# Optimization experiments

Hardware: AMD Instinct MI355X
Metric: run time of the kernel (lower is better)

## Reference

```python
import jax, jax.numpy as jnp
import numpy as np

B, C, N = 8, 512, 2048
C8 = C // 8


def setup_inputs() -> dict:
    key = jax.random.key(0)
    kx, kq, kk, kv, kg = jax.random.split(key, 5)
    return {
        "x": jax.random.normal(kx, (B, C, N), dtype=jnp.float32),
        "Wq": jax.random.normal(kq, (C8, C), dtype=jnp.float32) * (1.0 / np.sqrt(C)),
        "Wk": jax.random.normal(kk, (C8, C), dtype=jnp.float32) * (1.0 / np.sqrt(C)),
        "Wv": jax.random.normal(kv, (C, C), dtype=jnp.float32) * (1.0 / np.sqrt(C)),
        # torch init is gamma=0.0; use a small random value so the attention
        # branch contributes to the output.
        "gamma": jax.random.uniform(kg, (1,), dtype=jnp.float32),
    }


def reference(x, Wq, Wk, Wv, gamma):
    # 1x1 convs == per-position linear maps over channels
    f = jnp.einsum("oc,bcn->bon", Wq, x)   # [B, C/8, N]
    g = jnp.einsum("oc,bcn->bon", Wk, x)   # [B, C/8, N]
    h = jnp.einsum("oc,bcn->bon", Wv, x)   # [B, C,   N]
    # scores[b,n,m] = sum_c f[b,c,n] * g[b,c,m]  (unscaled, as in source)
    scores = jnp.einsum("bcn,bcm->bnm", f, g)  # [B, N, N]
    # softmax over dim=1 (the query-position axis) — atypical but faithful
    beta = jax.nn.softmax(scores, axis=1)
    # o = gamma * h @ beta + x
    o = gamma[0] * jnp.einsum("bcn,bnm->bcm", h, beta) + x
    return o
```

## Files before the change

### kernel.cpp

```cpp
#include <hip/hip_runtime.h>
#include <hip/hip_bf16.h>
#include <math.h>

#define NB 8
#define NC 512
#define NN 2048

typedef unsigned short u16;
typedef __attribute__((ext_vector_type(8))) short short8;
typedef __attribute__((ext_vector_type(4))) float f32x4;

__device__ __forceinline__ float bf16_to_f32(u16 v) {
  union { unsigned int u; float f; } c; c.u = ((unsigned int)v) << 16; return c.f;
}
__device__ __forceinline__ u16 f32_to_bf16(float f) {
  __hip_bfloat16 h = __float2bfloat16(f);
  union { __hip_bfloat16 h; u16 u; } c; c.h = h; return c.u;
}
__device__ __forceinline__ void split2(float v, unsigned short& hi, unsigned short& lo) {
  hi = f32_to_bf16(v);
  lo = f32_to_bf16(v - bf16_to_f32(hi));
}

__device__ __forceinline__ void gl_lds16(const void* g, void* l) {
  __builtin_amdgcn_global_load_lds(
      (const __attribute__((address_space(1))) unsigned int*)g,
      (__attribute__((address_space(3))) unsigned int*)l, 16, 0, 0);
}

__device__ __forceinline__ void stage128x32(const u16* __restrict__ src, size_t row_base,
                                            int selems, int k0, u16* lds, int tid) {
#pragma unroll
  for (int s = 0; s < 2; ++s) {
    int flat = s * 4096 + tid * 16;
    int row = flat >> 6;
    int kb  = flat & 63;
    const char* g = (const char*)(src + (row_base + row) * (size_t)selems + k0) + kb;
    u16* l = lds + s * 2048 + (tid & ~63) * 8;
    gl_lds16(g, l);
  }
}

__global__ __launch_bounds__(256)
void wsplit_kernel(const float* __restrict__ Wq, const float* __restrict__ Wk,
                   const float* __restrict__ Wv, u16* __restrict__ Whi,
                   u16* __restrict__ Wlo) {
  int idx = (blockIdx.x * 256 + threadIdx.x) * 4;
  int r = idx >> 9, c = idx & 511;
  const float* src;
  if (r < 64)       src = Wq + (size_t)r * NC + c;
  else if (r < 128) src = Wk + (size_t)(r - 64) * NC + c;
  else              src = Wv + (size_t)(r - 128) * NC + c;
  float4 v = *(const float4*)src;
  ushort4 hi, lo;
  split2(v.x, hi.x, lo.x); split2(v.y, hi.y, lo.y);
  split2(v.z, hi.z, lo.z); split2(v.w, hi.w, lo.w);
  *(ushort4*)&Whi[idx] = hi;
  *(ushort4*)&Wlo[idx] = lo;
}

__global__ __launch_bounds__(256)
void xsplit_kernel(const float* __restrict__ x, u16* __restrict__ xThi,
                   u16* __restrict__ xTlo) {
  const int b = blockIdx.z, c0 = blockIdx.y * 64, n0 = blockIdx.x * 64;
  __shared__ float t[64][65];
  const int tid = threadIdx.x, tx = tid & 15, ty = tid >> 4;
#pragma unroll
  for (int r = 0; r < 4; ++r) {
    int c = r * 16 + ty;
    float4 v = *(const float4*)&x[((size_t)b * NC + c0 + c) * NN + n0 + tx * 4];
    t[c][tx * 4 + 0] = v.x; t[c][tx * 4 + 1] = v.y;
    t[c][tx * 4 + 2] = v.z; t[c][tx * 4 + 3] = v.w;
  }
  __syncthreads();
#pragma unroll
  for (int r = 0; r < 4; ++r) {
    int n = r * 16 + ty;
    ushort4 hi, lo;
    split2(t[tx * 4 + 0][n], hi.x, lo.x);
    split2(t[tx * 4 + 1][n], hi.y, lo.y);
    split2(t[tx * 4 + 2][n], hi.z, lo.z);
    split2(t[tx * 4 + 3][n], hi.w, lo.w);
    size_t off = ((size_t)b * NN + n0 + n) * NC + c0 + tx * 4;
    *(ushort4*)&xThi[off] = hi;
    *(ushort4*)&xTlo[off] = lo;
  }
}

__global__ __launch_bounds__(256)
void proj_mfma_kernel(const u16* __restrict__ xThi, const u16* __restrict__ xTlo,
                      const u16* __restrict__ Whi, const u16* __restrict__ Wlo,
                      u16* __restrict__ fgThi, u16* __restrict__ fgTlo,
                      u16* __restrict__ hw) {
  const int b  = blockIdx.z;
  const int n0 = blockIdx.x * 128;
  const int r0 = blockIdx.y * 128;
  const bool fg = (r0 == 0);

  __shared__ u16 Wh[2][128 * 32], Wl[2][128 * 32], Xh[2][128 * 32], Xl[2][128 * 32];

  const int tid = threadIdx.x, wave = tid >> 6, lane = tid & 63;
  const int quad = lane >> 4, l16 = lane & 15;
  const int wa = (wave >> 1) * 64, wb = (wave & 1) * 64;
  const size_t xrow = (size_t)b * NN + n0;

  f32x4 acc[4][4];
#pragma unroll
  for (int i = 0; i < 4; ++i)
#pragma unroll
    for (int j = 0; j < 4; ++j) acc[i][j] = (f32x4){0.f, 0.f, 0.f, 0.f};

  stage128x32(Whi, r0, NC, 0, Wh[0], tid);
  stage128x32(xThi, xrow, NC, 0, Xh[0], tid);
  if (fg) {
    stage128x32(Wlo, r0, NC, 0, Wl[0], tid);
    stage128x32(xTlo, xrow, NC, 0, Xl[0], tid);
  }

  const int KIT = NC / 32;
  for (int ki = 0; ki < KIT; ++ki) {
    __syncthreads();
    if (ki + 1 < KIT) {
      const int nb = (ki + 1) & 1, k1 = (ki + 1) * 32;
      stage128x32(Whi, r0, NC, k1, Wh[nb], tid);
      stage128x32(xThi, xrow, NC, k1, Xh[nb], tid);
      if (fg) {
        stage128x32(Wlo, r0, NC, k1, Wl[nb], tid);
        stage128x32(xTlo, xrow, NC, k1, Xl[nb], tid);
      }
    }
    const int cur = ki & 1;

    if (fg) {
      short8 ah[4], al[4], bh[4], bl[4];
#pragma unroll
      for (int i = 0; i < 4; ++i) {
        ah[i] = *(short8*)&Wh[cur][(wa + i * 16 + l16) * 32 + quad * 8];
        al[i] = *(short8*)&Wl[cur][(wa + i * 16 + l16) * 32 + quad * 8];
      }
#pragma unroll
      for (int j = 0; j < 4; ++j) {
        bh[j] = *(short8*)&Xh[cur][(wb + j * 16 + l16) * 32 + quad * 8];
        bl[j] = *(short8*)&Xl[cur][(wb + j * 16 + l16) * 32 + quad * 8];
      }
#pragma unroll
      for (int i = 0; i < 4; ++i)
#pragma unroll
        for (int j = 0; j < 4; ++j) {
          acc[i][j] = __builtin_amdgcn_mfma_f32_16x16x32_bf16(ah[i], bh[j], acc[i][j], 0, 0, 0);
          acc[i][j] = __builtin_amdgcn_mfma_f32_16x16x32_bf16(ah[i], bl[j], acc[i][j], 0, 0, 0);
          acc[i][j] = __builtin_amdgcn_mfma_f32_16x16x32_bf16(al[i], bh[j], acc[i][j], 0, 0, 0);
        }
    } else {
      short8 ah[4], bh[4];
#pragma unroll
      for (int i = 0; i < 4; ++i)
        ah[i] = *(short8*)&Xh[cur][(wa + i * 16 + l16) * 32 + quad * 8];
#pragma unroll
      for (int j = 0; j < 4; ++j)
        bh[j] = *(short8*)&Wh[cur][(wb + j * 16 + l16) * 32 + quad * 8];
#pragma unroll
      for (int i = 0; i < 4; ++i)
#pragma unroll
        for (int j = 0; j < 4; ++j)
          acc[i][j] = __builtin_amdgcn_mfma_f32_16x16x32_bf16(ah[i], bh[j], acc[i][j], 0, 0, 0);
    }
  }

  if (fg) {
#pragma unroll
    for (int i = 0; i < 4; ++i)
#pragma unroll
      for (int j = 0; j < 4; ++j) {
        int rb = wa + i * 16 + quad * 4;
        int n  = n0 + wb + j * 16 + l16;
        ushort4 hi, lo;
        split2(acc[i][j][0], hi.x, lo.x); split2(acc[i][j][1], hi.y, lo.y);
        split2(acc[i][j][2], hi.z, lo.z); split2(acc[i][j][3], hi.w, lo.w);
        size_t off = ((size_t)b * NN + n) * 128 + rb;
        *(ushort4*)&fgThi[off] = hi;
        *(ushort4*)&fgTlo[off] = lo;
      }
  } else {
#pragma unroll
    for (int i = 0; i < 4; ++i)
#pragma unroll
      for (int j = 0; j < 4; ++j) {
        int nb = n0 + wa + i * 16 + quad * 4;
        int c  = r0 - 128 + wb + j * 16 + l16;
        ushort4 hi;
        hi.x = f32_to_bf16(acc[i][j][0]); hi.y = f32_to_bf16(acc[i][j][1]);
        hi.z = f32_to_bf16(acc[i][j][2]); hi.w = f32_to_bf16(acc[i][j][3]);
        *(ushort4*)&hw[((size_t)b * NC + c) * NN + nb] = hi;
      }
  }
}

__global__ __launch_bounds__(512, 2)
void attn_out_kernel(const u16* __restrict__ fgThi, const u16* __restrict__ fgTlo,
                     const u16* __restrict__ hw, const float* __restrict__ x,
                     const float* __restrict__ gamma, float* __restrict__ out) {
  const int s = blockIdx.x;
  const int b = s & 7;
  const int mt = s >> 3;
  const int m0 = mt * 64;

  __shared__ u16 Fh[2][64 * 64], Fl[2][64 * 64];
  __shared__ u16 Ps[64 * 64];
  float* Dn = (float*)Ps;

  const int tid = threadIdx.x, wave = tid >> 6, lane = tid & 63;
  const int quad = lane >> 4, l16 = lane & 15;
  const int ws_n = (wave >> 2) * 32, ws_m = (wave & 3) * 16;
  const int wv_c = wave * 64;

  const size_t frow = (size_t)b * NN;
  const size_t hbase = (size_t)b * NC;

  short8 gh[2], gl[2];
#pragma unroll
  for (int k = 0; k < 2; ++k) {
    size_t o = (frow + m0 + ws_m + l16) * 128 + 64 + k * 32 + quad * 8;
    gh[k] = *(const short8*)&fgThi[o];
    gl[k] = *(const short8*)&fgTlo[o];
  }

  {
    int flat = tid * 16;
    int row = flat >> 7, chunk = (flat >> 4) & 7;
    int kb = ((chunk ^ (row & 7)) << 4);
    gl_lds16((const char*)(fgThi + (frow + row) * 128) + kb, Fh[0] + (tid & ~63) * 8);
    gl_lds16((const char*)(fgTlo + (frow + row) * 128) + kb, Fl[0] + (tid & ~63) * 8);
  }
  __syncthreads();

  float dsum = 0.f;
  f32x4 ao[4][4];
#pragma unroll
  for (int i = 0; i < 4; ++i)
#pragma unroll
    for (int j = 0; j < 4; ++j) ao[i][j] = (f32x4){0.f, 0.f, 0.f, 0.f};

  const int NT = NN / 64;
  for (int it = 0; it < NT; ++it) {
    const int cur = it & 1;
    const int n1 = it * 64;

    short8 hreg[8];
#pragma unroll
    for (int i = 0; i < 4; ++i)
#pragma unroll
      for (int k = 0; k < 2; ++k)
        hreg[i * 2 + k] = *(const short8*)&hw[
            (hbase + wv_c + i * 16 + l16) * NN + n1 + (k * 4 + quad) * 8];

    if (it + 1 < NT) {
      const int nf = (it + 1) * 64;
      int flat = tid * 16;
      int row = flat >> 7, chunk = (flat >> 4) & 7;
      int kb = ((chunk ^ (row & 7)) << 4);
      gl_lds16((const char*)(fgThi + (frow + nf + row) * 128) + kb,
               Fh[cur ^ 1] + (tid & ~63) * 8);
      gl_lds16((const char*)(fgTlo + (frow + nf + row) * 128) + kb,
               Fl[cur ^ 1] + (tid & ~63) * 8);
    }

    f32x4 as[2];
#pragma unroll
    for (int i = 0; i < 2; ++i) as[i] = (f32x4){0.f, 0.f, 0.f, 0.f};
#pragma unroll
    for (int k = 0; k < 2; ++k) {
      short8 fh[2], fl[2];
#pragma unroll
      for (int i = 0; i < 2; ++i) {
        int rr = ws_n + i * 16 + l16;
        int ci = (((k * 4 + quad) ^ (rr & 7)) << 3);
        fh[i] = *(short8*)&Fh[cur][rr * 64 + ci];
        fl[i] = *(short8*)&Fl[cur][rr * 64 + ci];
      }
#pragma unroll
      for (int i = 0; i < 2; ++i) {
        as[i] = __builtin_amdgcn_mfma_f32_16x16x32_bf16(fh[i], gh[k], as[i], 0, 0, 0);
        as[i] = __builtin_amdgcn_mfma_f32_16x16x32_bf16(fh[i], gl[k], as[i], 0, 0, 0);
        as[i] = __builtin_amdgcn_mfma_f32_16x16x32_bf16(fl[i], gh[k], as[i], 0, 0, 0);
      }
    }

    {
      int m = ws_m + l16;
#pragma unroll
      for (int i = 0; i < 2; ++i) {
        float e0 = __expf(as[i][0]);
        float e1 = __expf(as[i][1]);
        float e2 = __expf(as[i][2]);
        float e3 = __expf(as[i][3]);
        dsum += (e0 + e1) + (e2 + e3);
        ushort4 pk;
        pk.x = f32_to_bf16(e0); pk.y = f32_to_bf16(e1);
        pk.z = f32_to_bf16(e2); pk.w = f32_to_bf16(e3);
        int nb = ws_n * 2 + i * 32 + quad * 8;
        int chunk = nb >> 4;
        int off = (nb & 15) >> 1;
        *(ushort4*)&Ps[m * 64 + ((chunk ^ (m & 7)) << 3) + off] = pk;
      }
    }

    asm volatile("s_waitcnt lgkmcnt(0)" ::: "memory");
    __builtin_amdgcn_s_barrier();

#pragma unroll
    for (int k = 0; k < 2; ++k) {
      short8 pb[4];
#pragma unroll
      for (int j = 0; j < 4; ++j) {
        int rm = j * 16 + l16;
        pb[j] = *(short8*)&Ps[rm * 64 + ((((k * 4 + quad)) ^ (rm & 7)) << 3)];
      }
#pragma unroll
      for (int i = 0; i < 4; ++i)
#pragma unroll
        for (int j = 0; j < 4; ++j)
          ao[i][j] = __builtin_amdgcn_mfma_f32_16x16x32_bf16(hreg[i * 2 + k], pb[j], ao[i][j], 0, 0, 0);
    }

    __syncthreads();
  }

  dsum += __shfl_xor(dsum, 16);
  dsum += __shfl_xor(dsum, 32);
  if (tid < 64) Dn[tid] = 0.f;
  __syncthreads();
  if (quad == 0) atomicAdd(&Dn[ws_m + l16], dsum);
  __syncthreads();

  const float g = gamma[0];
  float invd[4];
#pragma unroll
  for (int j = 0; j < 4; ++j)
    invd[j] = g / Dn[j * 16 + l16];

#pragma unroll
  for (int i = 0; i < 4; ++i) {
#pragma unroll
    for (int j = 0; j < 4; ++j) {
      const int c = wv_c + i * 16 + quad * 4;
      const int m = m0 + j * 16 + l16;
#pragma unroll
      for (int r = 0; r < 4; ++r) {
        size_t off = ((size_t)b * NC + c + r) * NN + m;
        out[off] = fmaf(invd[j], ao[i][j][r], x[off]);
      }
    }
  }
}

extern "C" void kernel_launch(void* const* d_in, const int* in_sizes, int n_in,
                              void* d_out, int out_size, void* d_ws, size_t ws_size,
                              hipStream_t stream) {
  const float* x     = (const float*)d_in[0];
  const float* Wq    = (const float*)d_in[1];
  const float* Wk    = (const float*)d_in[2];
  const float* Wv    = (const float*)d_in[3];
  const float* gamma = (const float*)d_in[4];
  float* out = (float*)d_out;

  char* ws = (char*)d_ws;
  u16*   xThi  = (u16*)ws;
  u16*   xTlo  = (u16*)(ws + 16777216);
  u16*   Whi   = (u16*)(ws + 33554432);
  u16*   Wlo   = (u16*)(ws + 34209792);
  u16*   fgThi = (u16*)(ws + 67108864);
  u16*   fgTlo = (u16*)(ws + 71303168);
  u16*   hw    = (u16*)(ws + 75497472);

  wsplit_kernel<<<dim3(320), 256, 0, stream>>>(Wq, Wk, Wv, Whi, Wlo);
  xsplit_kernel<<<dim3(NN / 64, NC / 64, NB), 256, 0, stream>>>(x, xThi, xTlo);
  proj_mfma_kernel<<<dim3(NN / 128, 5, NB), 256, 0, stream>>>(
      xThi, xTlo, Whi, Wlo, fgThi, fgTlo, hw);
  attn_out_kernel<<<dim3(256), 512, 0, stream>>>(fgThi, fgTlo, hw, x, gamma, out);
}
```

Before: 224.0 us.

## Halve attention output tile to 32 columns and double grid size

The attention-output kernel now processes 32 output positions per block instead of 64 and launches 512 blocks instead of 256. Wave roles in the score computation are remapped so each wave computes one 16x16 score tile. The launch-bounds occupancy hint is raised to 4 blocks per CU. The aim is to fill more CUs and hide latency, at the cost of reloading the full F tiles and H rows twice as often per output column, which doubles global traffic for those operands.

```diff
diff --git a/kernel.cpp b/kernel.cpp
--- a/kernel.cpp
+++ b/kernel.cpp
@@ -196,22 +196,22 @@
   }
 }
 
-__global__ __launch_bounds__(512, 2)
+__global__ __launch_bounds__(512, 4)
 void attn_out_kernel(const u16* __restrict__ fgThi, const u16* __restrict__ fgTlo,
                      const u16* __restrict__ hw, const float* __restrict__ x,
                      const float* __restrict__ gamma, float* __restrict__ out) {
   const int s = blockIdx.x;
   const int b = s & 7;
   const int mt = s >> 3;
-  const int m0 = mt * 64;
+  const int m0 = mt * 32;
 
   __shared__ u16 Fh[2][64 * 64], Fl[2][64 * 64];
-  __shared__ u16 Ps[64 * 64];
-  float* Dn = (float*)Ps;
+  __shared__ u16 Ps[32 * 64];
+  __shared__ float Dn[32];
 
   const int tid = threadIdx.x, wave = tid >> 6, lane = tid & 63;
   const int quad = lane >> 4, l16 = lane & 15;
-  const int ws_n = (wave >> 2) * 32, ws_m = (wave & 3) * 16;
+  const int ws_n = (wave >> 1) * 16, ws_m = (wave & 1) * 16;
   const int wv_c = wave * 64;
 
   const size_t frow = (size_t)b * NN;
@@ -235,11 +235,11 @@
   __syncthreads();
 
   float dsum = 0.f;
-  f32x4 ao[4][4];
+  f32x4 ao[4][2];
 #pragma unroll
   for (int i = 0; i < 4; ++i)
 #pragma unroll
-    for (int j = 0; j < 4; ++j) ao[i][j] = (f32x4){0.f, 0.f, 0.f, 0.f};
+    for (int j = 0; j < 2; ++j) ao[i][j] = (f32x4){0.f, 0.f, 0.f, 0.f};
 
   const int NT = NN / 64;
   for (int it = 0; it < NT; ++it) {
@@ -265,44 +265,32 @@
                Fl[cur ^ 1] + (tid & ~63) * 8);
     }
 
-    f32x4 as[2];
-#pragma unroll
-    for (int i = 0; i < 2; ++i) as[i] = (f32x4){0.f, 0.f, 0.f, 0.f};
+    f32x4 as = (f32x4){0.f, 0.f, 0.f, 0.f};
 #pragma unroll
     for (int k = 0; k < 2; ++k) {
-      short8 fh[2], fl[2];
-#pragma unroll
-      for (int i = 0; i < 2; ++i) {
-        int rr = ws_n + i * 16 + l16;
-        int ci = (((k * 4 + quad) ^ (rr & 7)) << 3);
-        fh[i] = *(short8*)&Fh[cur][rr * 64 + ci];
-        fl[i] = *(short8*)&Fl[cur][rr * 64 + ci];
-      }
-#pragma unroll
-      for (int i = 0; i < 2; ++i) {
-        as[i] = __builtin_amdgcn_mfma_f32_16x16x32_bf16(fh[i], gh[k], as[i], 0, 0, 0);
-        as[i] = __builtin_amdgcn_mfma_f32_16x16x32_bf16(fh[i], gl[k], as[i], 0, 0, 0);
-        as[i] = __builtin_amdgcn_mfma_f32_16x16x32_bf16(fl[i], gh[k], as[i], 0, 0, 0);
-      }
+      int rr = ws_n + l16;
+      int ci = (((k * 4 + quad) ^ (rr & 7)) << 3);
+      short8 fh = *(short8*)&Fh[cur][rr * 64 + ci];
+      short8 fl = *(short8*)&Fl[cur][rr * 64 + ci];
+      as = __builtin_amdgcn_mfma_f32_16x16x32_bf16(fh, gh[k], as, 0, 0, 0);
+      as = __builtin_amdgcn_mfma_f32_16x16x32_bf16(fh, gl[k], as, 0, 0, 0);
+      as = __builtin_amdgcn_mfma_f32_16x16x32_bf16(fl, gh[k], as, 0, 0, 0);
     }
 
     {
       int m = ws_m + l16;
-#pragma unroll
-      for (int i = 0; i < 2; ++i) {
-        float e0 = __expf(as[i][0]);
-        float e1 = __expf(as[i][1]);
-        float e2 = __expf(as[i][2]);
-        float e3 = __expf(as[i][3]);
-        dsum += (e0 + e1) + (e2 + e3);
-        ushort4 pk;
-        pk.x = f32_to_bf16(e0); pk.y = f32_to_bf16(e1);
-        pk.z = f32_to_bf16(e2); pk.w = f32_to_bf16(e3);
-        int nb = ws_n * 2 + i * 32 + quad * 8;
-        int chunk = nb >> 4;
-        int off = (nb & 15) >> 1;
-        *(ushort4*)&Ps[m * 64 + ((chunk ^ (m & 7)) << 3) + off] = pk;
-      }
+      float e0 = __expf(as[0]);
+      float e1 = __expf(as[1]);
+      float e2 = __expf(as[2]);
+      float e3 = __expf(as[3]);
+      dsum += (e0 + e1) + (e2 + e3);
+      ushort4 pk;
+      pk.x = f32_to_bf16(e0); pk.y = f32_to_bf16(e1);
+      pk.z = f32_to_bf16(e2); pk.w = f32_to_bf16(e3);
+      int nb = ws_n * 2 + quad * 8;
+      int chunk = nb >> 4;
+      int off = (nb & 15) >> 1;
+      *(ushort4*)&Ps[m * 64 + ((chunk ^ (m & 7)) << 3) + off] = pk;
     }
 
     asm volatile("s_waitcnt lgkmcnt(0)" ::: "memory");
@@ -310,16 +298,16 @@
 
 #pragma unroll
     for (int k = 0; k < 2; ++k) {
-      short8 pb[4];
-#pragma unroll
-      for (int j = 0; j < 4; ++j) {
+      short8 pb[2];
+#pragma unroll
+      for (int j = 0; j < 2; ++j) {
         int rm = j * 16 + l16;
         pb[j] = *(short8*)&Ps[rm * 64 + ((((k * 4 + quad)) ^ (rm & 7)) << 3)];
       }
 #pragma unroll
       for (int i = 0; i < 4; ++i)
 #pragma unroll
-        for (int j = 0; j < 4; ++j)
+        for (int j = 0; j < 2; ++j)
           ao[i][j] = __builtin_amdgcn_mfma_f32_16x16x32_bf16(hreg[i * 2 + k], pb[j], ao[i][j], 0, 0, 0);
     }
 
@@ -328,21 +316,21 @@
 
   dsum += __shfl_xor(dsum, 16);
   dsum += __shfl_xor(dsum, 32);
-  if (tid < 64) Dn[tid] = 0.f;
+  if (tid < 32) Dn[tid] = 0.f;
   __syncthreads();
   if (quad == 0) atomicAdd(&Dn[ws_m + l16], dsum);
   __syncthreads();
 
   const float g = gamma[0];
-  float invd[4];
-#pragma unroll
-  for (int j = 0; j < 4; ++j)
+  float invd[2];
+#pragma unroll
+  for (int j = 0; j < 2; ++j)
     invd[j] = g / Dn[j * 16 + l16];
 
 #pragma unroll
   for (int i = 0; i < 4; ++i) {
 #pragma unroll
-    for (int j = 0; j < 4; ++j) {
+    for (int j = 0; j < 2; ++j) {
       const int c = wv_c + i * 16 + quad * 4;
       const int m = m0 + j * 16 + l16;
 #pragma unroll
@@ -377,5 +365,5 @@
   xsplit_kernel<<<dim3(NN / 64, NC / 64, NB), 256, 0, stream>>>(x, xThi, xTlo);
   proj_mfma_kernel<<<dim3(NN / 128, 5, NB), 256, 0, stream>>>(
       xThi, xTlo, Whi, Wlo, fgThi, fgTlo, hw);
-  attn_out_kernel<<<dim3(256), 512, 0, stream>>>(fgThi, fgTlo, hw, x, gamma, out);
-}
+  attn_out_kernel<<<dim3(512), 512, 0, stream>>>(fgThi, fgTlo, hw, x, gamma, out);
+}
```

Result: slower. 265.0 us (+18.3%).
